# Optimization experiments

Hardware: AMD Instinct MI355X
Metric: run time of the kernel (lower is better)

Reference implementation:

```python
import jax, jax.numpy as jnp
import numpy as np

N = 20000
E = 320000
IN_CH = 512
OUT_CH = 256


def setup_inputs() -> dict:
    key = jax.random.key(0)
    ks = jax.random.split(key, 24)
    p = lambda k, shape: jax.random.normal(k, shape, jnp.float32) * 0.05
    return {
        "x": jax.random.normal(ks[0], (N, IN_CH), jnp.float32),
        "edge_index": jax.random.randint(ks[1], (2, E), 0, N),
        "original_size": 16384,
        "W1": p(ks[2], (IN_CH, 4 * 256)), "as1": p(ks[3], (4, 256)), "ad1": p(ks[4], (4, 256)), "b1": p(ks[5], (1024,)),
        "lw1": p(ks[6], (IN_CH, 1024)), "lb1": p(ks[7], (1024,)),
        "W2": p(ks[8], (1024, 4 * 256)), "as2": p(ks[9], (4, 256)), "ad2": p(ks[10], (4, 256)), "b2": p(ks[11], (1024,)),
        "lw2": p(ks[12], (1024, 1024)), "lb2": p(ks[13], (1024,)),
        "W3": p(ks[14], (1024, 6 * 256)), "as3": p(ks[15], (6, 256)), "ad3": p(ks[16], (6, 256)), "b3": p(ks[17], (256,)),
        "lw3": p(ks[18], (1024, OUT_CH)), "lb3": p(ks[19], (OUT_CH,)),
    }


def gat_conv(x, src, dst, W, a_src, a_dst, bias, heads, ch, concat):
    """PyG-style GATConv: gather -> edge attention -> segment softmax -> scatter-add."""
    n = x.shape[0]
    h = (x @ W).reshape(n, heads, ch)                      # [N,H,C]
    alpha_s = (h * a_src[None]).sum(-1)                    # [N,H]
    alpha_d = (h * a_dst[None]).sum(-1)                    # [N,H]
    e = jax.nn.leaky_relu(alpha_s[src] + alpha_d[dst], 0.2)  # [E,H]
    m = jax.ops.segment_max(e, dst, num_segments=n)        # per-dst max (stable softmax)
    e = jnp.exp(e - m[dst])
    denom = jax.ops.segment_sum(e, dst, num_segments=n)
    alpha = e / (denom[dst] + 1e-16)                       # [E,H]
    msg = h[src] * alpha[:, :, None]                       # [E,H,C]
    out = jax.ops.segment_sum(msg, dst, num_segments=n)    # [N,H,C]
    out = out.reshape(n, heads * ch) if concat else out.mean(axis=1)
    return out + bias


def reference(x, edge_index, original_size, W1, as1, ad1, b1, lw1, lb1,
              W2, as2, ad2, b2, lw2, lb2, W3, as3, ad3, b3, lw3, lb3):
    n = x.shape[0]
    loops = jnp.arange(n)
    src = jnp.concatenate([edge_index[0], loops])  # PyG add_self_loops=True default
    dst = jnp.concatenate([edge_index[1], loops])
    h = jax.nn.elu(gat_conv(x, src, dst, W1, as1, ad1, b1, 4, 256, True) + x @ lw1 + lb1)
    h = jax.nn.elu(gat_conv(h, src, dst, W2, as2, ad2, b2, 4, 256, True) + h @ lw2 + lb2)
    h = gat_conv(h, src, dst, W3, as3, ad3, b3, 6, 256, False) + h @ lw3 + lb3
    return h[:original_size]
```

## Files before the change

### kernel.cpp

```cpp
#include <hip/hip_runtime.h>

#define N_NODES 20000
#define M_PAD   20096
#define E_EDGES 320000

typedef unsigned short u16;
typedef unsigned int   u32;
typedef __attribute__((ext_vector_type(8))) short bf16x8;
typedef __attribute__((ext_vector_type(4))) float f32x4;

__device__ __forceinline__ float bf2f(u16 u){
  u32 x = ((u32)u) << 16; float f; __builtin_memcpy(&f, &x, 4); return f;
}
__device__ __forceinline__ u16 f2bf(float f){
  u32 u; __builtin_memcpy(&u, &f, 4);
  u += 0x7fffu + ((u >> 16) & 1u);
  return (u16)(u >> 16);
}

__device__ __forceinline__ void gl_lds16(const void* g, void* l){
  __builtin_amdgcn_global_load_lds((const __attribute__((address_space(1))) void*)g,
                                   (__attribute__((address_space(3))) void*)l, 16, 0, 0);
}

__global__ void hist_k(const int* __restrict__ ei, int* __restrict__ cnt){
  int i = blockIdx.x * 256 + threadIdx.x;
  if (i < E_EDGES) atomicAdd(&cnt[ei[E_EDGES + i]], 1);
}

__global__ void scan_k(const int* __restrict__ cnt, int* __restrict__ rowp, int n){
  __shared__ int wsum[16], wpre[16];
  __shared__ int carry;
  int tid = threadIdx.x, lane = tid & 63, wv = tid >> 6;
  if (tid == 0) carry = 0;
  __syncthreads();
  for (int base = 0; base < n; base += 1024){
    int i = base + tid;
    int v = (i < n) ? cnt[i] : 0;
    int incl = v;
#pragma unroll
    for (int d = 1; d < 64; d <<= 1){
      int t = __shfl_up(incl, d, 64);
      if (lane >= d) incl += t;
    }
    if (lane == 63) wsum[wv] = incl;
    __syncthreads();
    if (tid == 0){
      int s = carry;
#pragma unroll
      for (int w = 0; w < 16; w++){ wpre[w] = s; s += wsum[w]; }
      carry = s;
    }
    __syncthreads();
    if (i < n) rowp[i] = wpre[wv] + incl - v;
  }
  __syncthreads();
  if (tid == 0) rowp[n] = carry;
}

__global__ void copy_int_k(const int* __restrict__ a, int* __restrict__ b, int n){
  int i = blockIdx.x * 256 + threadIdx.x; if (i < n) b[i] = a[i];
}

__global__ void scatter_k(const int* __restrict__ ei, int* __restrict__ fill, int* __restrict__ esrc){
  int i = blockIdx.x * 256 + threadIdx.x;
  if (i < E_EDGES){
    int d = ei[E_EDGES + i];
    int p = atomicAdd(&fill[d], 1);
    esrc[p] = ei[i];
  }
}

__global__ void tcast_k(const float* __restrict__ src, int Nc, u16* __restrict__ dst, int n0, int ldd){
  __shared__ float tile[32][33];
  int kb = blockIdx.y * 32, nb = blockIdx.x * 32;
  int tx = threadIdx.x, ty = threadIdx.y;
#pragma unroll
  for (int r = 0; r < 32; r += 8)
    tile[ty + r][tx] = src[(size_t)(kb + ty + r) * Nc + nb + tx];
  __syncthreads();
#pragma unroll
  for (int r = 0; r < 32; r += 8){
    int n = nb + ty + r;
    dst[(size_t)(n0 + n) * ldd + kb + tx] = f2bf(tile[tx][ty + r]);
  }
}

__global__ void castx_k(const float* __restrict__ x, u16* __restrict__ o, int realRows){
  int r = blockIdx.x, c = threadIdx.x * 2;
  float2 v = (r < realRows) ? *(const float2*)(x + (size_t)r * 512 + c) : make_float2(0.f, 0.f);
  u32 pk = ((u32)f2bf(v.y) << 16) | (u32)f2bf(v.x);
  *(u32*)(o + (size_t)r * 512 + c) = pk;
}

__global__ void zpad_k(u16* __restrict__ p, int n){
  int i = blockIdx.x * 256 + threadIdx.x; if (i < n) p[i] = 0;
}

__global__ __launch_bounds__(256, 2)
void gemm_bf16(const u16* __restrict__ A, const u16* __restrict__ Bt, u16* __restrict__ C,
               int N, int K)
{
  __shared__ __attribute__((aligned(16))) u16 lA[128 * 32];
  __shared__ __attribute__((aligned(16))) u16 lB[256 * 32];
  const int tid  = threadIdx.x;
  const int wave = tid >> 6, lane = tid & 63;
  const int bn = blockIdx.x, bm = blockIdx.y;
  const int wm = (wave >> 1) * 64, wn = (wave & 1) * 128;

  const int srow  = wave * 16 + (lane >> 2);
  const int skcol = (lane & 3) * 8;
  const u16* Ag0 = A  + (size_t)(bm * 128 + srow) * K + skcol;
  const u16* Ag1 = Ag0 + (size_t)64 * K;
  const u16* Bg  = Bt + (size_t)(bn * 256 + srow) * K + skcol;
  u16* lA0 = lA + wave * 512; u16* lA1 = lA + 2048 + wave * 512;
  u16* lBw = lB + wave * 512;

  f32x4 acc[4][8] = {};

  for (int k0 = 0; k0 < K; k0 += 32){
    gl_lds16(Ag0 + k0, lA0);
    gl_lds16(Ag1 + k0, lA1);
#pragma unroll
    for (int c = 0; c < 4; c++)
      gl_lds16(Bg + (size_t)(c * 64) * K + k0, lBw + c * 2048);
    __syncthreads();
    const int koff = (lane >> 4) * 8;
    const int rsel = lane & 15;
    bf16x8 af[4], bfr[8];
#pragma unroll
    for (int i = 0; i < 4; i++) af[i]  = *(const bf16x8*)&lA[(wm + i * 16 + rsel) * 32 + koff];
#pragma unroll
    for (int j = 0; j < 8; j++) bfr[j] = *(const bf16x8*)&lB[(wn + j * 16 + rsel) * 32 + koff];
#pragma unroll
    for (int i = 0; i < 4; i++)
#pragma unroll
      for (int j = 0; j < 8; j++)
        acc[i][j] = __builtin_amdgcn_mfma_f32_16x16x32_bf16(af[i], bfr[j], acc[i][j], 0, 0, 0);
    __syncthreads();
  }

  const int r0 = (lane >> 4) * 4, cl = lane & 15;
#pragma unroll
  for (int i = 0; i < 4; i++)
#pragma unroll
    for (int j = 0; j < 8; j++){
      int row = bm * 128 + wm + i * 16 + r0;
      int col = bn * 256 + wn + j * 16 + cl;
      u16* cp = C + (size_t)row * N + col;
#pragma unroll
      for (int r = 0; r < 4; r++) cp[(size_t)r * N] = f2bf(acc[i][j][r]);
    }
}

__global__ void alpha_k(const u16* __restrict__ HG, int ldH,
                        const float* __restrict__ a_s, const float* __restrict__ a_d,
                        float* __restrict__ aS, float* __restrict__ aD, int H)
{
  int n = blockIdx.x, h = blockIdx.y, lane = threadIdx.x;
  const u16* rp = HG + (size_t)n * ldH + h * 256 + lane * 4;
  ushort4 u = *(const ushort4*)rp;
  float4 av = *(const float4*)(a_s + h * 256 + lane * 4);
  float4 dv = *(const float4*)(a_d + h * 256 + lane * 4);
  float x0 = bf2f(u.x), x1 = bf2f(u.y), x2 = bf2f(u.z), x3 = bf2f(u.w);
  float s = x0 * av.x + x1 * av.y + x2 * av.z + x3 * av.w;
  float d = x0 * dv.x + x1 * dv.y + x2 * dv.z + x3 * dv.w;
#pragma unroll
  for (int off = 32; off; off >>= 1){ s += __shfl_down(s, off); d += __shfl_down(d, off); }
  if (lane == 0){ aS[(size_t)n * H + h] = s; aD[(size_t)n * H + h] = d; }
}

template<int H, bool FINAL>
__global__ __launch_bounds__(256)
void agg_k(const u16* __restrict__ HG, int ldH,
           const int* __restrict__ rowp, const int* __restrict__ esrc,
           const float* __restrict__ aS, const float* __restrict__ aD,
           const float* __restrict__ bias, const float* __restrict__ lbias,
           int gatCols, u16* __restrict__ outb, int ldo, float* __restrict__ outf)
{
  constexpr int PERT = H;
  constexpr int MAXE = 320;
  __shared__ float s_m[H], s_dinv[H], s_red[4 * H];
  __shared__ float s_ew[MAXE * H];
  __shared__ int   s_src[MAXE];
  __shared__ float s_fin[FINAL ? 1536 : 4];

  const int dst = blockIdx.x;
  const int tid = threadIdx.x, lane = tid & 63, wv = tid >> 6;
  const int e0 = rowp[dst];
  const int deg = rowp[dst + 1] - e0;
  const int nE = deg + 1;
  const bool fits = (nE <= MAXE);

  float adv[H];
#pragma unroll
  for (int h = 0; h < H; h++) adv[h] = aD[(size_t)dst * H + h];

  float lm[H];
#pragma unroll
  for (int h = 0; h < H; h++) lm[h] = -1e30f;
  for (int i = tid; i < nE; i += 256){
    int s = (i == deg) ? dst : esrc[e0 + i];
    if (fits) s_src[i] = s;
#pragma unroll
    for (int h = 0; h < H; h++){
      float e = aS[(size_t)s * H + h] + adv[h];
      e = e > 0.f ? e : 0.2f * e;
      if (fits) s_ew[i * H + h] = e;
      lm[h] = fmaxf(lm[h], e);
    }
  }
#pragma unroll
  for (int h = 0; h < H; h++)
#pragma unroll
    for (int off = 32; off; off >>= 1) lm[h] = fmaxf(lm[h], __shfl_down(lm[h], off));
  if (lane == 0){
#pragma unroll
    for (int h = 0; h < H; h++) s_red[wv * H + h] = lm[h];
  }
  __syncthreads();
  if (tid < H) s_m[tid] = fmaxf(fmaxf(s_red[tid], s_red[H + tid]),
                                fmaxf(s_red[2 * H + tid], s_red[3 * H + tid]));
  __syncthreads();

  float ls[H];
#pragma unroll
  for (int h = 0; h < H; h++) ls[h] = 0.f;
  for (int i = tid; i < nE; i += 256){
    if (fits){
#pragma unroll
      for (int h = 0; h < H; h++){
        float w = __expf(s_ew[i * H + h] - s_m[h]);
        s_ew[i * H + h] = w;
        ls[h] += w;
      }
    } else {
      int s = (i == deg) ? dst : esrc[e0 + i];
#pragma unroll
      for (int h = 0; h < H; h++){
        float e = aS[(size_t)s * H + h] + adv[h];
        e = e > 0.f ? e : 0.2f * e;
        ls[h] += __expf(e - s_m[h]);
      }
    }
  }
#pragma unroll
  for (int h = 0; h < H; h++)
#pragma unroll
    for (int off = 32; off; off >>= 1) ls[h] += __shfl_down(ls[h], off);
  if (lane == 0){
#pragma unroll
    for (int h = 0; h < H; h++) s_red[wv * H + h] = ls[h];
  }
  __syncthreads();
  if (tid < H) s_dinv[tid] = 1.f / (s_red[tid] + s_red[H + tid] + s_red[2 * H + tid] + s_red[3 * H + tid] + 1e-16f);
  __syncthreads();

  float acc[PERT];
#pragma unroll
  for (int c = 0; c < PERT; c++) acc[c] = 0.f;
  const int ch0 = tid * PERT;

  if constexpr (H == 4){
    const int hh = tid >> 6;
    const float dinv = s_dinv[hh];
    const u16* HGb = HG + ch0;
    if (fits){
      int i = 0;
      for (; i + 2 <= nE; i += 2){
        int s0 = s_src[i], s1 = s_src[i + 1];
        float w0 = s_ew[i * 4 + hh] * dinv;
        float w1 = s_ew[i * 4 + 4 + hh] * dinv;
        ushort4 u0 = *(const ushort4*)(HGb + (size_t)s0 * ldH);
        ushort4 u1 = *(const ushort4*)(HGb + (size_t)s1 * ldH);
        acc[0] += w0 * bf2f(u0.x) + w1 * bf2f(u1.x);
        acc[1] += w0 * bf2f(u0.y) + w1 * bf2f(u1.y);
        acc[2] += w0 * bf2f(u0.z) + w1 * bf2f(u1.z);
        acc[3] += w0 * bf2f(u0.w) + w1 * bf2f(u1.w);
      }
      if (i < nE){
        int s0 = s_src[i];
        float w0 = s_ew[i * 4 + hh] * dinv;
        ushort4 u0 = *(const ushort4*)(HGb + (size_t)s0 * ldH);
        acc[0] += w0 * bf2f(u0.x); acc[1] += w0 * bf2f(u0.y);
        acc[2] += w0 * bf2f(u0.z); acc[3] += w0 * bf2f(u0.w);
      }
    } else {
      for (int i = 0; i < nE; i++){
        int s = (i == deg) ? dst : esrc[e0 + i];
        float e = aS[(size_t)s * 4 + hh] + adv[hh];
        e = e > 0.f ? e : 0.2f * e;
        float w = __expf(e - s_m[hh]) * dinv;
        ushort4 u = *(const ushort4*)(HGb + (size_t)s * ldH);
        acc[0] += w * bf2f(u.x); acc[1] += w * bf2f(u.y);
        acc[2] += w * bf2f(u.z); acc[3] += w * bf2f(u.w);
      }
    }
  } else {
    const int h0 = ch0 >> 8;
    const int h1 = (ch0 + 5) >> 8;
    const float dinv0 = s_dinv[h0], dinv1 = s_dinv[h1];
    const int bnd = (h0 + 1) * 256;
    const u32* HGb = (const u32*)HG;
    const int rowd = ldH >> 1;
    if (fits){
      int i = 0;
      for (; i + 2 <= nE; i += 2){
        int s0 = s_src[i], s1 = s_src[i + 1];
        float p0 = s_ew[i * 6 + h0] * dinv0, q0 = s_ew[i * 6 + h1] * dinv1;
        float p1 = s_ew[i * 6 + 6 + h0] * dinv0, q1 = s_ew[i * 6 + 6 + h1] * dinv1;
        const u32* r0p = HGb + (size_t)s0 * rowd + tid * 3;
        const u32* r1p = HGb + (size_t)s1 * rowd + tid * 3;
        u32 a0 = r0p[0], a1 = r0p[1], a2 = r0p[2];
        u32 b0 = r1p[0], b1 = r1p[1], b2 = r1p[2];
        float v0[6] = { bf2f((u16)(a0 & 0xffff)), bf2f((u16)(a0 >> 16)),
                        bf2f((u16)(a1 & 0xffff)), bf2f((u16)(a1 >> 16)),
                        bf2f((u16)(a2 & 0xffff)), bf2f((u16)(a2 >> 16)) };
        float v1[6] = { bf2f((u16)(b0 & 0xffff)), bf2f((u16)(b0 >> 16)),
                        bf2f((u16)(b1 & 0xffff)), bf2f((u16)(b1 >> 16)),
                        bf2f((u16)(b2 & 0xffff)), bf2f((u16)(b2 >> 16)) };
#pragma unroll
        for (int c = 0; c < 6; c++){
          bool lo = (ch0 + c) < bnd;
          acc[c] += (lo ? p0 : q0) * v0[c] + (lo ? p1 : q1) * v1[c];
        }
      }
      if (i < nE){
        int s0 = s_src[i];
        float p0 = s_ew[i * 6 + h0] * dinv0, q0 = s_ew[i * 6 + h1] * dinv1;
        const u32* r0p = HGb + (size_t)s0 * rowd + tid * 3;
        u32 a0 = r0p[0], a1 = r0p[1], a2 = r0p[2];
        float v0[6] = { bf2f((u16)(a0 & 0xffff)), bf2f((u16)(a0 >> 16)),
                        bf2f((u16)(a1 & 0xffff)), bf2f((u16)(a1 >> 16)),
                        bf2f((u16)(a2 & 0xffff)), bf2f((u16)(a2 >> 16)) };
#pragma unroll
        for (int c = 0; c < 6; c++) acc[c] += (((ch0 + c) < bnd) ? p0 : q0) * v0[c];
      }
    } else {
      for (int i = 0; i < nE; i++){
        int s = (i == deg) ? dst : esrc[e0 + i];
        float ea = aS[(size_t)s * 6 + h0] + adv[h0];
        ea = ea > 0.f ? ea : 0.2f * ea;
        float p0 = __expf(ea - s_m[h0]) * dinv0;
        float eb = aS[(size_t)s * 6 + h1] + adv[h1];
        eb = eb > 0.f ? eb : 0.2f * eb;
        float q0 = __expf(eb - s_m[h1]) * dinv1;
        const u32* r0p = HGb + (size_t)s * rowd + tid * 3;
        u32 a0 = r0p[0], a1 = r0p[1], a2 = r0p[2];
        float v0[6] = { bf2f((u16)(a0 & 0xffff)), bf2f((u16)(a0 >> 16)),
                        bf2f((u16)(a1 & 0xffff)), bf2f((u16)(a1 >> 16)),
                        bf2f((u16)(a2 & 0xffff)), bf2f((u16)(a2 >> 16)) };
#pragma unroll
        for (int c = 0; c < 6; c++) acc[c] += (((ch0 + c) < bnd) ? p0 : q0) * v0[c];
      }
    }
  }

  if constexpr (FINAL){
#pragma unroll
    for (int c = 0; c < PERT; c++) s_fin[ch0 + c] = acc[c];
    __syncthreads();
    int c = tid;
    float v = 0.f;
#pragma unroll
    for (int h = 0; h < 6; h++) v += s_fin[h * 256 + c];
    v = v * (1.f / 6.f) + bias[c] + bf2f(HG[(size_t)dst * ldH + gatCols + c]) + lbias[c];
    outf[(size_t)dst * 256 + c] = v;
  } else {
    const u16* lr = HG + (size_t)dst * ldH + gatCols;
    ushort4 u = *(const ushort4*)(lr + ch0);
    float lv[4] = { bf2f(u.x), bf2f(u.y), bf2f(u.z), bf2f(u.w) };
    ushort4 o;
    float v0 = acc[0] + bias[ch0 + 0] + lv[0] + lbias[ch0 + 0]; v0 = v0 > 0.f ? v0 : __expf(v0) - 1.f;
    float v1 = acc[1] + bias[ch0 + 1] + lv[1] + lbias[ch0 + 1]; v1 = v1 > 0.f ? v1 : __expf(v1) - 1.f;
    float v2 = acc[2] + bias[ch0 + 2] + lv[2] + lbias[ch0 + 2]; v2 = v2 > 0.f ? v2 : __expf(v2) - 1.f;
    float v3 = acc[3] + bias[ch0 + 3] + lv[3] + lbias[ch0 + 3]; v3 = v3 > 0.f ? v3 : __expf(v3) - 1.f;
    o.x = f2bf(v0); o.y = f2bf(v1); o.z = f2bf(v2); o.w = f2bf(v3);
    *(ushort4*)(outb + (size_t)dst * ldo + ch0) = o;
  }
}

extern "C" void kernel_launch(void* const* d_in, const int* in_sizes, int n_in,
                              void* d_out, int out_size, void* d_ws, size_t ws_size,
                              hipStream_t stream)
{
  const float* x   = (const float*)d_in[0];
  const int*   ei  = (const int*)  d_in[1];
  const float* W1  = (const float*)d_in[3];
  const float* as1 = (const float*)d_in[4];
  const float* ad1 = (const float*)d_in[5];
  const float* b1  = (const float*)d_in[6];
  const float* lw1 = (const float*)d_in[7];
  const float* lb1 = (const float*)d_in[8];
  const float* W2  = (const float*)d_in[9];
  const float* as2 = (const float*)d_in[10];
  const float* ad2 = (const float*)d_in[11];
  const float* b2  = (const float*)d_in[12];
  const float* lw2 = (const float*)d_in[13];
  const float* lb2 = (const float*)d_in[14];
  const float* W3  = (const float*)d_in[15];
  const float* as3 = (const float*)d_in[16];
  const float* ad3 = (const float*)d_in[17];
  const float* b3  = (const float*)d_in[18];
  const float* lw3 = (const float*)d_in[19];
  const float* lb3 = (const float*)d_in[20];

  char* wp = (char*)d_ws;
  auto nxt = [&](size_t b) -> void* {
    void* p = (void*)wp; wp += (b + 255) & ~(size_t)255; return p;
  };
  u16*  Wt1  = (u16*) nxt((size_t)2048 * 512  * 2);
  u16*  Wt2  = (u16*) nxt((size_t)2048 * 1024 * 2);
  u16*  Wt3  = (u16*) nxt((size_t)1792 * 1024 * 2);
  u16*  Xb   = (u16*) nxt((size_t)M_PAD * 1024 * 2);
  u16*  HG   = (u16*) nxt((size_t)M_PAD * 2048 * 2);
  float* aS  = (float*)nxt((size_t)N_NODES * 6 * 4);
  float* aD  = (float*)nxt((size_t)N_NODES * 6 * 4);
  int*  cnt  = (int*)  nxt((size_t)N_NODES * 4);
  int*  rowp = (int*)  nxt((size_t)(N_NODES + 1) * 4);
  int*  fill = (int*)  nxt((size_t)N_NODES * 4);
  int*  esrc = (int*)  nxt((size_t)E_EDGES * 4);

  hipMemsetAsync(cnt, 0, (size_t)N_NODES * 4, stream);
  hist_k   <<<(E_EDGES + 255) / 256, 256, 0, stream>>>(ei, cnt);
  scan_k   <<<1, 1024, 0, stream>>>(cnt, rowp, N_NODES);
  copy_int_k<<<(N_NODES + 255) / 256, 256, 0, stream>>>(rowp, fill, N_NODES);
  scatter_k<<<(E_EDGES + 255) / 256, 256, 0, stream>>>(ei, fill, esrc);

  dim3 tb(32, 8);
  tcast_k<<<dim3(1024 / 32, 512  / 32), tb, 0, stream>>>(W1,  1024, Wt1, 0,    512);
  tcast_k<<<dim3(1024 / 32, 512  / 32), tb, 0, stream>>>(lw1, 1024, Wt1, 1024, 512);
  tcast_k<<<dim3(1024 / 32, 1024 / 32), tb, 0, stream>>>(W2,  1024, Wt2, 0,    1024);
  tcast_k<<<dim3(1024 / 32, 1024 / 32), tb, 0, stream>>>(lw2, 1024, Wt2, 1024, 1024);
  tcast_k<<<dim3(1536 / 32, 1024 / 32), tb, 0, stream>>>(W3,  1536, Wt3, 0,    1024);
  tcast_k<<<dim3(256  / 32, 1024 / 32), tb, 0, stream>>>(lw3, 256,  Wt3, 1536, 1024);

  castx_k<<<M_PAD, 256, 0, stream>>>(x, Xb, N_NODES);
  zpad_k <<<(96 * 1024 + 255) / 256, 256, 0, stream>>>(Xb + (size_t)N_NODES * 1024, 96 * 1024);

  const int MT = M_PAD / 128;

  gemm_bf16<<<dim3(2048 / 256, MT), 256, 0, stream>>>(Xb, Wt1, HG, 2048, 512);
  alpha_k  <<<dim3(N_NODES, 4), 64, 0, stream>>>(HG, 2048, as1, ad1, aS, aD, 4);
  agg_k<4, false><<<N_NODES, 256, 0, stream>>>(HG, 2048, rowp, esrc, aS, aD, b1, lb1, 1024, Xb, 1024, nullptr);

  gemm_bf16<<<dim3(2048 / 256, MT), 256, 0, stream>>>(Xb, Wt2, HG, 2048, 1024);
  alpha_k  <<<dim3(N_NODES, 4), 64, 0, stream>>>(HG, 2048, as2, ad2, aS, aD, 4);
  agg_k<4, false><<<N_NODES, 256, 0, stream>>>(HG, 2048, rowp, esrc, aS, aD, b2, lb2, 1024, Xb, 1024, nullptr);

  gemm_bf16<<<dim3(1792 / 256, MT), 256, 0, stream>>>(Xb, Wt3, HG, 1792, 1024);
  alpha_k  <<<dim3(N_NODES, 6), 64, 0, stream>>>(HG, 1792, as3, ad3, aS, aD, 6);
  int outRows = out_size / 256;
  agg_k<6, true><<<outRows, 256, 0, stream>>>(HG, 1792, rowp, esrc, aS, aD, b3, lb3, 1536, nullptr, 0, (float*)d_out);

  (void)in_sizes; (void)n_in; (void)ws_size;
}
```

Baseline: 909.1 us.

## Fuse attention-logit dot products into GEMM epilogue and widen aggregation loads

The separate alpha kernel is removed. Attention logits are now computed in the GEMM epilogue from the fp32 accumulators, using a cross-lane shuffle reduction and an LDS combine across waves. The aggregation kernels are rewritten so each thread loads 16-byte chunks of 8 bf16 channels, and two edge groups per block combine partial sums through shared memory. A 384-thread variant handles the six-head layer. The weight transpose launches and the copy kernel are merged into one tcast kernel and the scan, cutting launch count. The GEMM epilogue gains extra LDS work and syncs, and logits now come from unrounded fp32 accumulators rather than bf16-stored values.

```diff
diff --git a/kernel.cpp b/kernel.cpp
--- a/kernel.cpp
+++ b/kernel.cpp
@@ -8,6 +8,7 @@
 typedef unsigned int   u32;
 typedef __attribute__((ext_vector_type(8))) short bf16x8;
 typedef __attribute__((ext_vector_type(4))) float f32x4;
+typedef __attribute__((ext_vector_type(4))) u32   u32x4;
 
 __device__ __forceinline__ float bf2f(u16 u){
   u32 x = ((u32)u) << 16; float f; __builtin_memcpy(&f, &x, 4); return f;
@@ -23,12 +24,22 @@
                                    (__attribute__((address_space(3))) void*)l, 16, 0, 0);
 }
 
+__device__ __forceinline__ void acc8(float* acc, float w, u32x4 p){
+#pragma unroll
+  for (int d = 0; d < 4; d++){
+    u32 u = p[d];
+    acc[2 * d]     += w * bf2f((u16)(u & 0xffff));
+    acc[2 * d + 1] += w * bf2f((u16)(u >> 16));
+  }
+}
+
 __global__ void hist_k(const int* __restrict__ ei, int* __restrict__ cnt){
   int i = blockIdx.x * 256 + threadIdx.x;
   if (i < E_EDGES) atomicAdd(&cnt[ei[E_EDGES + i]], 1);
 }
 
-__global__ void scan_k(const int* __restrict__ cnt, int* __restrict__ rowp, int n){
+__global__ void scan_k(const int* __restrict__ cnt, int* __restrict__ rowp,
+                       int* __restrict__ fill, int n){
   __shared__ int wsum[16], wpre[16];
   __shared__ int carry;
   int tid = threadIdx.x, lane = tid & 63, wv = tid >> 6;
@@ -52,14 +63,10 @@
       carry = s;
     }
     __syncthreads();
-    if (i < n) rowp[i] = wpre[wv] + incl - v;
+    if (i < n){ int e = wpre[wv] + incl - v; rowp[i] = e; fill[i] = e; }
   }
   __syncthreads();
   if (tid == 0) rowp[n] = carry;
-}
-
-__global__ void copy_int_k(const int* __restrict__ a, int* __restrict__ b, int n){
-  int i = blockIdx.x * 256 + threadIdx.x; if (i < n) b[i] = a[i];
 }
 
 __global__ void scatter_k(const int* __restrict__ ei, int* __restrict__ fill, int* __restrict__ esrc){
@@ -71,9 +78,21 @@
   }
 }
 
-__global__ void tcast_k(const float* __restrict__ src, int Nc, u16* __restrict__ dst, int n0, int ldd){
+__global__ void tcast_all(const float* __restrict__ W1, const float* __restrict__ lw1, u16* __restrict__ Wt1,
+                          const float* __restrict__ W2, const float* __restrict__ lw2, u16* __restrict__ Wt2,
+                          const float* __restrict__ W3, const float* __restrict__ lw3, u16* __restrict__ Wt3)
+{
   __shared__ float tile[32][33];
-  int kb = blockIdx.y * 32, nb = blockIdx.x * 32;
+  int b = blockIdx.x;
+  const float* src; u16* dst; int Nc, n0, ldd;
+  if      (b <  512){            src = W1;  Nc = 1024; dst = Wt1; n0 = 0;    ldd = 512;  }
+  else if (b < 1024){ b -=  512; src = lw1; Nc = 1024; dst = Wt1; n0 = 1024; ldd = 512;  }
+  else if (b < 2048){ b -= 1024; src = W2;  Nc = 1024; dst = Wt2; n0 = 0;    ldd = 1024; }
+  else if (b < 3072){ b -= 2048; src = lw2; Nc = 1024; dst = Wt2; n0 = 1024; ldd = 1024; }
+  else if (b < 4608){ b -= 3072; src = W3;  Nc = 1536; dst = Wt3; n0 = 0;    ldd = 1024; }
+  else              { b -= 4608; src = lw3; Nc = 256;  dst = Wt3; n0 = 1536; ldd = 1024; }
+  int gx = Nc / 32;
+  int kb = (b / gx) * 32, nb = (b % gx) * 32;
   int tx = threadIdx.x, ty = threadIdx.y;
 #pragma unroll
   for (int r = 0; r < 32; r += 8)
@@ -99,7 +118,9 @@
 
 __global__ __launch_bounds__(256, 2)
 void gemm_bf16(const u16* __restrict__ A, const u16* __restrict__ Bt, u16* __restrict__ C,
-               int N, int K)
+               int N, int K,
+               const float* __restrict__ a_s, const float* __restrict__ a_d,
+               float* __restrict__ aS, float* __restrict__ aD, int H)
 {
   __shared__ __attribute__((aligned(16))) u16 lA[128 * 32];
   __shared__ __attribute__((aligned(16))) u16 lB[256 * 32];
@@ -151,39 +172,58 @@
 #pragma unroll
       for (int r = 0; r < 4; r++) cp[(size_t)r * N] = f2bf(acc[i][j][r]);
     }
-}
-
-__global__ void alpha_k(const u16* __restrict__ HG, int ldH,
-                        const float* __restrict__ a_s, const float* __restrict__ a_d,
-                        float* __restrict__ aS, float* __restrict__ aD, int H)
+
+  if (bn < H){
+    float* fa = (float*)lA;
+    fa[tid]       = a_s[bn * 256 + tid];
+    fa[256 + tid] = a_d[bn * 256 + tid];
+    __syncthreads();
+    float* fb = (float*)lB;
+    const int q = lane >> 4;
+#pragma unroll
+    for (int i = 0; i < 4; i++)
+#pragma unroll
+      for (int r = 0; r < 4; r++){
+        float ps = 0.f, pd = 0.f;
+#pragma unroll
+        for (int j = 0; j < 8; j++){
+          float v = acc[i][j][r];
+          int c = wn + j * 16 + cl;
+          ps += v * fa[c];
+          pd += v * fa[256 + c];
+        }
+#pragma unroll
+        for (int m = 1; m < 16; m <<= 1){
+          ps += __shfl_xor(ps, m, 64);
+          pd += __shfl_xor(pd, m, 64);
+        }
+        if (cl == 0){
+          int row = wm + i * 16 + q * 4 + r;
+          fb[(wave & 1) * 128 + row]       = ps;
+          fb[256 + (wave & 1) * 128 + row] = pd;
+        }
+      }
+    __syncthreads();
+    if (tid < 128){
+      int row = bm * 128 + tid;
+      aS[(size_t)row * H + bn] = fb[tid] + fb[128 + tid];
+      aD[(size_t)row * H + bn] = fb[256 + tid] + fb[384 + tid];
+    }
+  }
+}
+
+__global__ __launch_bounds__(256)
+void agg4_k(const u16* __restrict__ HG, int ldH,
+            const int* __restrict__ rowp, const int* __restrict__ esrc,
+            const float* __restrict__ aS, const float* __restrict__ aD,
+            const float* __restrict__ bias, const float* __restrict__ lbias,
+            u16* __restrict__ outb)
 {
-  int n = blockIdx.x, h = blockIdx.y, lane = threadIdx.x;
-  const u16* rp = HG + (size_t)n * ldH + h * 256 + lane * 4;
-  ushort4 u = *(const ushort4*)rp;
-  float4 av = *(const float4*)(a_s + h * 256 + lane * 4);
-  float4 dv = *(const float4*)(a_d + h * 256 + lane * 4);
-  float x0 = bf2f(u.x), x1 = bf2f(u.y), x2 = bf2f(u.z), x3 = bf2f(u.w);
-  float s = x0 * av.x + x1 * av.y + x2 * av.z + x3 * av.w;
-  float d = x0 * dv.x + x1 * dv.y + x2 * dv.z + x3 * dv.w;
-#pragma unroll
-  for (int off = 32; off; off >>= 1){ s += __shfl_down(s, off); d += __shfl_down(d, off); }
-  if (lane == 0){ aS[(size_t)n * H + h] = s; aD[(size_t)n * H + h] = d; }
-}
-
-template<int H, bool FINAL>
-__global__ __launch_bounds__(256)
-void agg_k(const u16* __restrict__ HG, int ldH,
-           const int* __restrict__ rowp, const int* __restrict__ esrc,
-           const float* __restrict__ aS, const float* __restrict__ aD,
-           const float* __restrict__ bias, const float* __restrict__ lbias,
-           int gatCols, u16* __restrict__ outb, int ldo, float* __restrict__ outf)
-{
-  constexpr int PERT = H;
   constexpr int MAXE = 320;
-  __shared__ float s_m[H], s_dinv[H], s_red[4 * H];
-  __shared__ float s_ew[MAXE * H];
+  __shared__ float s_m[4], s_dinv[4], s_red[16];
+  __shared__ float s_ew[MAXE * 4];
   __shared__ int   s_src[MAXE];
-  __shared__ float s_fin[FINAL ? 1536 : 4];
+  __shared__ float s_acc[2][1024];
 
   const int dst = blockIdx.x;
   const int tid = threadIdx.x, lane = tid & 63, wv = tid >> 6;
@@ -192,191 +232,259 @@
   const int nE = deg + 1;
   const bool fits = (nE <= MAXE);
 
-  float adv[H];
-#pragma unroll
-  for (int h = 0; h < H; h++) adv[h] = aD[(size_t)dst * H + h];
-
-  float lm[H];
-#pragma unroll
-  for (int h = 0; h < H; h++) lm[h] = -1e30f;
+  float4 adv = *(const float4*)(aD + (size_t)dst * 4);
+
+  float lm[4] = { -1e30f, -1e30f, -1e30f, -1e30f };
   for (int i = tid; i < nE; i += 256){
     int s = (i == deg) ? dst : esrc[e0 + i];
     if (fits) s_src[i] = s;
-#pragma unroll
-    for (int h = 0; h < H; h++){
-      float e = aS[(size_t)s * H + h] + adv[h];
-      e = e > 0.f ? e : 0.2f * e;
-      if (fits) s_ew[i * H + h] = e;
-      lm[h] = fmaxf(lm[h], e);
-    }
-  }
-#pragma unroll
-  for (int h = 0; h < H; h++)
+    float4 as = *(const float4*)(aS + (size_t)s * 4);
+    float e0h = as.x + adv.x; e0h = e0h > 0.f ? e0h : 0.2f * e0h;
+    float e1h = as.y + adv.y; e1h = e1h > 0.f ? e1h : 0.2f * e1h;
+    float e2h = as.z + adv.z; e2h = e2h > 0.f ? e2h : 0.2f * e2h;
+    float e3h = as.w + adv.w; e3h = e3h > 0.f ? e3h : 0.2f * e3h;
+    if (fits){ s_ew[i*4+0]=e0h; s_ew[i*4+1]=e1h; s_ew[i*4+2]=e2h; s_ew[i*4+3]=e3h; }
+    lm[0] = fmaxf(lm[0], e0h); lm[1] = fmaxf(lm[1], e1h);
+    lm[2] = fmaxf(lm[2], e2h); lm[3] = fmaxf(lm[3], e3h);
+  }
+#pragma unroll
+  for (int h = 0; h < 4; h++)
 #pragma unroll
     for (int off = 32; off; off >>= 1) lm[h] = fmaxf(lm[h], __shfl_down(lm[h], off));
   if (lane == 0){
 #pragma unroll
-    for (int h = 0; h < H; h++) s_red[wv * H + h] = lm[h];
-  }
-  __syncthreads();
-  if (tid < H) s_m[tid] = fmaxf(fmaxf(s_red[tid], s_red[H + tid]),
-                                fmaxf(s_red[2 * H + tid], s_red[3 * H + tid]));
-  __syncthreads();
-
-  float ls[H];
-#pragma unroll
-  for (int h = 0; h < H; h++) ls[h] = 0.f;
+    for (int h = 0; h < 4; h++) s_red[wv * 4 + h] = lm[h];
+  }
+  __syncthreads();
+  if (tid < 4) s_m[tid] = fmaxf(fmaxf(s_red[tid], s_red[4 + tid]),
+                                fmaxf(s_red[8 + tid], s_red[12 + tid]));
+  __syncthreads();
+
+  float ls[4] = {0.f, 0.f, 0.f, 0.f};
   for (int i = tid; i < nE; i += 256){
     if (fits){
 #pragma unroll
-      for (int h = 0; h < H; h++){
-        float w = __expf(s_ew[i * H + h] - s_m[h]);
-        s_ew[i * H + h] = w;
+      for (int h = 0; h < 4; h++){
+        float w = __expf(s_ew[i * 4 + h] - s_m[h]);
+        s_ew[i * 4 + h] = w;
         ls[h] += w;
       }
     } else {
       int s = (i == deg) ? dst : esrc[e0 + i];
-#pragma unroll
-      for (int h = 0; h < H; h++){
-        float e = aS[(size_t)s * H + h] + adv[h];
+      float4 as = *(const float4*)(aS + (size_t)s * 4);
+      float e;
+      e = as.x + adv.x; e = e > 0.f ? e : 0.2f * e; ls[0] += __expf(e - s_m[0]);
+      e = as.y + adv.y; e = e > 0.f ? e : 0.2f * e; ls[1] += __expf(e - s_m[1]);
+      e = as.z + adv.z; e = e > 0.f ? e : 0.2f * e; ls[2] += __expf(e - s_m[2]);
+      e = as.w + adv.w; e = e > 0.f ? e : 0.2f * e; ls[3] += __expf(e - s_m[3]);
+    }
+  }
+#pragma unroll
+  for (int h = 0; h < 4; h++)
+#pragma unroll
+    for (int off = 32; off; off >>= 1) ls[h] += __shfl_down(ls[h], off);
+  if (lane == 0){
+#pragma unroll
+    for (int h = 0; h < 4; h++) s_red[wv * 4 + h] = ls[h];
+  }
+  __syncthreads();
+  if (tid < 4) s_dinv[tid] = 1.f / (s_red[tid] + s_red[4 + tid] + s_red[8 + tid] + s_red[12 + tid] + 1e-16f);
+  __syncthreads();
+
+  const int grp = wv >> 1;
+  const int ch0 = (wv & 1) * 512 + lane * 8;
+  const int h   = ch0 >> 8;
+  const float dinv = s_dinv[h];
+  const float mh   = s_m[h];
+  float acc[8] = {};
+  const u16* HGb = HG + ch0;
+
+  if (fits){
+    int i = grp;
+    for (; i + 2 < nE; i += 4){
+      int s0 = s_src[i], s1 = s_src[i + 2];
+      float w0 = s_ew[i * 4 + h] * dinv;
+      float w1 = s_ew[(i + 2) * 4 + h] * dinv;
+      u32x4 p0 = *(const u32x4*)(HGb + (size_t)s0 * ldH);
+      u32x4 p1 = *(const u32x4*)(HGb + (size_t)s1 * ldH);
+      acc8(acc, w0, p0);
+      acc8(acc, w1, p1);
+    }
+    if (i < nE){
+      int s0 = s_src[i];
+      float w0 = s_ew[i * 4 + h] * dinv;
+      u32x4 p0 = *(const u32x4*)(HGb + (size_t)s0 * ldH);
+      acc8(acc, w0, p0);
+    }
+  } else {
+    float advh = aD[(size_t)dst * 4 + h];
+    for (int i = grp; i < nE; i += 2){
+      int s = (i == deg) ? dst : esrc[e0 + i];
+      float e = aS[(size_t)s * 4 + h] + advh;
+      e = e > 0.f ? e : 0.2f * e;
+      float w = __expf(e - mh) * dinv;
+      u32x4 p = *(const u32x4*)(HGb + (size_t)s * ldH);
+      acc8(acc, w, p);
+    }
+  }
+#pragma unroll
+  for (int c = 0; c < 8; c++) s_acc[grp][ch0 + c] = acc[c];
+  __syncthreads();
+
+  const int c4 = tid * 4;
+  const u16* lr = HG + (size_t)dst * ldH + 1024 + c4;
+  ushort4 u = *(const ushort4*)lr;
+  float lv[4] = { bf2f(u.x), bf2f(u.y), bf2f(u.z), bf2f(u.w) };
+  ushort4 o;
+  float v0 = s_acc[0][c4+0] + s_acc[1][c4+0] + bias[c4+0] + lv[0] + lbias[c4+0]; v0 = v0 > 0.f ? v0 : __expf(v0) - 1.f;
+  float v1 = s_acc[0][c4+1] + s_acc[1][c4+1] + bias[c4+1] + lv[1] + lbias[c4+1]; v1 = v1 > 0.f ? v1 : __expf(v1) - 1.f;
+  float v2 = s_acc[0][c4+2] + s_acc[1][c4+2] + bias[c4+2] + lv[2] + lbias[c4+2]; v2 = v2 > 0.f ? v2 : __expf(v2) - 1.f;
+  float v3 = s_acc[0][c4+3] + s_acc[1][c4+3] + bias[c4+3] + lv[3] + lbias[c4+3]; v3 = v3 > 0.f ? v3 : __expf(v3) - 1.f;
+  o.x = f2bf(v0); o.y = f2bf(v1); o.z = f2bf(v2); o.w = f2bf(v3);
+  *(ushort4*)(outb + (size_t)dst * 1024 + c4) = o;
+}
+
+__global__ __launch_bounds__(384)
+void agg6_k(const u16* __restrict__ HG, int ldH,
+            const int* __restrict__ rowp, const int* __restrict__ esrc,
+            const float* __restrict__ aS, const float* __restrict__ aD,
+            const float* __restrict__ bias, const float* __restrict__ lbias,
+            float* __restrict__ outf)
+{
+  constexpr int MAXE = 320;
+  __shared__ float s_m[6], s_dinv[6], s_red[36];
+  __shared__ float s_ew[MAXE * 6];
+  __shared__ int   s_src[MAXE];
+  __shared__ float s_acc[2][1536];
+
+  const int dst = blockIdx.x;
+  const int tid = threadIdx.x, lane = tid & 63, wv = tid >> 6;
+  const int e0 = rowp[dst];
+  const int deg = rowp[dst + 1] - e0;
+  const int nE = deg + 1;
+  const bool fits = (nE <= MAXE);
+
+  float adv[6];
+#pragma unroll
+  for (int h = 0; h < 6; h++) adv[h] = aD[(size_t)dst * 6 + h];
+
+  float lm[6];
+#pragma unroll
+  for (int h = 0; h < 6; h++) lm[h] = -1e30f;
+  for (int i = tid; i < nE; i += 384){
+    int s = (i == deg) ? dst : esrc[e0 + i];
+    if (fits) s_src[i] = s;
+#pragma unroll
+    for (int h = 0; h < 6; h++){
+      float e = aS[(size_t)s * 6 + h] + adv[h];
+      e = e > 0.f ? e : 0.2f * e;
+      if (fits) s_ew[i * 6 + h] = e;
+      lm[h] = fmaxf(lm[h], e);
+    }
+  }
+#pragma unroll
+  for (int h = 0; h < 6; h++)
+#pragma unroll
+    for (int off = 32; off; off >>= 1) lm[h] = fmaxf(lm[h], __shfl_down(lm[h], off));
+  if (lane == 0){
+#pragma unroll
+    for (int h = 0; h < 6; h++) s_red[wv * 6 + h] = lm[h];
+  }
+  __syncthreads();
+  if (tid < 6){
+    float m = s_red[tid];
+#pragma unroll
+    for (int w = 1; w < 6; w++) m = fmaxf(m, s_red[w * 6 + tid]);
+    s_m[tid] = m;
+  }
+  __syncthreads();
+
+  float ls[6];
+#pragma unroll
+  for (int h = 0; h < 6; h++) ls[h] = 0.f;
+  for (int i = tid; i < nE; i += 384){
+    if (fits){
+#pragma unroll
+      for (int h = 0; h < 6; h++){
+        float w = __expf(s_ew[i * 6 + h] - s_m[h]);
+        s_ew[i * 6 + h] = w;
+        ls[h] += w;
+      }
+    } else {
+      int s = (i == deg) ? dst : esrc[e0 + i];
+#pragma unroll
+      for (int h = 0; h < 6; h++){
+        float e = aS[(size_t)s * 6 + h] + adv[h];
         e = e > 0.f ? e : 0.2f * e;
         ls[h] += __expf(e - s_m[h]);
       }
     }
   }
 #pragma unroll
-  for (int h = 0; h < H; h++)
+  for (int h = 0; h < 6; h++)
 #pragma unroll
     for (int off = 32; off; off >>= 1) ls[h] += __shfl_down(ls[h], off);
   if (lane == 0){
 #pragma unroll
-    for (int h = 0; h < H; h++) s_red[wv * H + h] = ls[h];
-  }
-  __syncthreads();
-  if (tid < H) s_dinv[tid] = 1.f / (s_red[tid] + s_red[H + tid] + s_red[2 * H + tid] + s_red[3 * H + tid] + 1e-16f);
-  __syncthreads();
-
-  float acc[PERT];
-#pragma unroll
-  for (int c = 0; c < PERT; c++) acc[c] = 0.f;
-  const int ch0 = tid * PERT;
-
-  if constexpr (H == 4){
-    const int hh = tid >> 6;
-    const float dinv = s_dinv[hh];
-    const u16* HGb = HG + ch0;
-    if (fits){
-      int i = 0;
-      for (; i + 2 <= nE; i += 2){
-        int s0 = s_src[i], s1 = s_src[i + 1];
-        float w0 = s_ew[i * 4 + hh] * dinv;
-        float w1 = s_ew[i * 4 + 4 + hh] * dinv;
-        ushort4 u0 = *(const ushort4*)(HGb + (size_t)s0 * ldH);
-        ushort4 u1 = *(const ushort4*)(HGb + (size_t)s1 * ldH);
-        acc[0] += w0 * bf2f(u0.x) + w1 * bf2f(u1.x);
-        acc[1] += w0 * bf2f(u0.y) + w1 * bf2f(u1.y);
-        acc[2] += w0 * bf2f(u0.z) + w1 * bf2f(u1.z);
-        acc[3] += w0 * bf2f(u0.w) + w1 * bf2f(u1.w);
-      }
-      if (i < nE){
-        int s0 = s_src[i];
-        float w0 = s_ew[i * 4 + hh] * dinv;
-        ushort4 u0 = *(const ushort4*)(HGb + (size_t)s0 * ldH);
-        acc[0] += w0 * bf2f(u0.x); acc[1] += w0 * bf2f(u0.y);
-        acc[2] += w0 * bf2f(u0.z); acc[3] += w0 * bf2f(u0.w);
-      }
-    } else {
-      for (int i = 0; i < nE; i++){
-        int s = (i == deg) ? dst : esrc[e0 + i];
-        float e = aS[(size_t)s * 4 + hh] + adv[hh];
-        e = e > 0.f ? e : 0.2f * e;
-        float w = __expf(e - s_m[hh]) * dinv;
-        ushort4 u = *(const ushort4*)(HGb + (size_t)s * ldH);
-        acc[0] += w * bf2f(u.x); acc[1] += w * bf2f(u.y);
-        acc[2] += w * bf2f(u.z); acc[3] += w * bf2f(u.w);
-      }
+    for (int h = 0; h < 6; h++) s_red[wv * 6 + h] = ls[h];
+  }
+  __syncthreads();
+  if (tid < 6){
+    float s = 0.f;
+#pragma unroll
+    for (int w = 0; w < 6; w++) s += s_red[w * 6 + tid];
+    s_dinv[tid] = 1.f / (s + 1e-16f);
+  }
+  __syncthreads();
+
+  const int grp  = wv / 3;
+  const int wrow = wv - grp * 3;
+  const int ch0  = wrow * 512 + lane * 8;
+  const int h    = ch0 >> 8;
+  const float dinv = s_dinv[h];
+  const float mh   = s_m[h];
+  float acc[8] = {};
+  const u16* HGb = HG + ch0;
+
+  if (fits){
+    int i = grp;
+    for (; i + 2 < nE; i += 4){
+      int s0 = s_src[i], s1 = s_src[i + 2];
+      float w0 = s_ew[i * 6 + h] * dinv;
+      float w1 = s_ew[(i + 2) * 6 + h] * dinv;
+      u32x4 p0 = *(const u32x4*)(HGb + (size_t)s0 * ldH);
+      u32x4 p1 = *(const u32x4*)(HGb + (size_t)s1 * ldH);
+      acc8(acc, w0, p0);
+      acc8(acc, w1, p1);
+    }
+    if (i < nE){
+      int s0 = s_src[i];
+      float w0 = s_ew[i * 6 + h] * dinv;
+      u32x4 p0 = *(const u32x4*)(HGb + (size_t)s0 * ldH);
+      acc8(acc, w0, p0);
     }
   } else {
-    const int h0 = ch0 >> 8;
-    const int h1 = (ch0 + 5) >> 8;
-    const float dinv0 = s_dinv[h0], dinv1 = s_dinv[h1];
-    const int bnd = (h0 + 1) * 256;
-    const u32* HGb = (const u32*)HG;
-    const int rowd = ldH >> 1;
-    if (fits){
-      int i = 0;
-      for (; i + 2 <= nE; i += 2){
-        int s0 = s_src[i], s1 = s_src[i + 1];
-        float p0 = s_ew[i * 6 + h0] * dinv0, q0 = s_ew[i * 6 + h1] * dinv1;
-        float p1 = s_ew[i * 6 + 6 + h0] * dinv0, q1 = s_ew[i * 6 + 6 + h1] * dinv1;
-        const u32* r0p = HGb + (size_t)s0 * rowd + tid * 3;
-        const u32* r1p = HGb + (size_t)s1 * rowd + tid * 3;
-        u32 a0 = r0p[0], a1 = r0p[1], a2 = r0p[2];
-        u32 b0 = r1p[0], b1 = r1p[1], b2 = r1p[2];
-        float v0[6] = { bf2f((u16)(a0 & 0xffff)), bf2f((u16)(a0 >> 16)),
-                        bf2f((u16)(a1 & 0xffff)), bf2f((u16)(a1 >> 16)),
-                        bf2f((u16)(a2 & 0xffff)), bf2f((u16)(a2 >> 16)) };
-        float v1[6] = { bf2f((u16)(b0 & 0xffff)), bf2f((u16)(b0 >> 16)),
-                        bf2f((u16)(b1 & 0xffff)), bf2f((u16)(b1 >> 16)),
-                        bf2f((u16)(b2 & 0xffff)), bf2f((u16)(b2 >> 16)) };
-#pragma unroll
-        for (int c = 0; c < 6; c++){
-          bool lo = (ch0 + c) < bnd;
-          acc[c] += (lo ? p0 : q0) * v0[c] + (lo ? p1 : q1) * v1[c];
-        }
-      }
-      if (i < nE){
-        int s0 = s_src[i];
-        float p0 = s_ew[i * 6 + h0] * dinv0, q0 = s_ew[i * 6 + h1] * dinv1;
-        const u32* r0p = HGb + (size_t)s0 * rowd + tid * 3;
-        u32 a0 = r0p[0], a1 = r0p[1], a2 = r0p[2];
-        float v0[6] = { bf2f((u16)(a0 & 0xffff)), bf2f((u16)(a0 >> 16)),
-                        bf2f((u16)(a1 & 0xffff)), bf2f((u16)(a1 >> 16)),
-                        bf2f((u16)(a2 & 0xffff)), bf2f((u16)(a2 >> 16)) };
-#pragma unroll
-        for (int c = 0; c < 6; c++) acc[c] += (((ch0 + c) < bnd) ? p0 : q0) * v0[c];
-      }
-    } else {
-      for (int i = 0; i < nE; i++){
-        int s = (i == deg) ? dst : esrc[e0 + i];
-        float ea = aS[(size_t)s * 6 + h0] + adv[h0];
-        ea = ea > 0.f ? ea : 0.2f * ea;
-        float p0 = __expf(ea - s_m[h0]) * dinv0;
-        float eb = aS[(size_t)s * 6 + h1] + adv[h1];
-        eb = eb > 0.f ? eb : 0.2f * eb;
-        float q0 = __expf(eb - s_m[h1]) * dinv1;
-        const u32* r0p = HGb + (size_t)s * rowd + tid * 3;
-        u32 a0 = r0p[0], a1 = r0p[1], a2 = r0p[2];
-        float v0[6] = { bf2f((u16)(a0 & 0xffff)), bf2f((u16)(a0 >> 16)),
-                        bf2f((u16)(a1 & 0xffff)), bf2f((u16)(a1 >> 16)),
-                        bf2f((u16)(a2 & 0xffff)), bf2f((u16)(a2 >> 16)) };
-#pragma unroll
-        for (int c = 0; c < 6; c++) acc[c] += (((ch0 + c) < bnd) ? p0 : q0) * v0[c];
-      }
-    }
-  }
-
-  if constexpr (FINAL){
-#pragma unroll
-    for (int c = 0; c < PERT; c++) s_fin[ch0 + c] = acc[c];
-    __syncthreads();
+    float advh = aD[(size_t)dst * 6 + h];
+    for (int i = grp; i < nE; i += 2){
+      int s = (i == deg) ? dst : esrc[e0 + i];
+      float e = aS[(size_t)s * 6 + h] + advh;
+      e = e > 0.f ? e : 0.2f * e;
+      float w = __expf(e - mh) * dinv;
+      u32x4 p = *(const u32x4*)(HGb + (size_t)s * ldH);
+      acc8(acc, w, p);
+    }
+  }
+#pragma unroll
+  for (int c = 0; c < 8; c++) s_acc[grp][ch0 + c] = acc[c];
+  __syncthreads();
+
+  if (tid < 256){
     int c = tid;
     float v = 0.f;
 #pragma unroll
-    for (int h = 0; h < 6; h++) v += s_fin[h * 256 + c];
-    v = v * (1.f / 6.f) + bias[c] + bf2f(HG[(size_t)dst * ldH + gatCols + c]) + lbias[c];
+    for (int hh = 0; hh < 6; hh++) v += s_acc[0][hh * 256 + c] + s_acc[1][hh * 256 + c];
+    v = v * (1.f / 6.f) + bias[c] + bf2f(HG[(size_t)dst * ldH + 1536 + c]) + lbias[c];
     outf[(size_t)dst * 256 + c] = v;
-  } else {
-    const u16* lr = HG + (size_t)dst * ldH + gatCols;
-    ushort4 u = *(const ushort4*)(lr + ch0);
-    float lv[4] = { bf2f(u.x), bf2f(u.y), bf2f(u.z), bf2f(u.w) };
-    ushort4 o;
-    float v0 = acc[0] + bias[ch0 + 0] + lv[0] + lbias[ch0 + 0]; v0 = v0 > 0.f ? v0 : __expf(v0) - 1.f;
-    float v1 = acc[1] + bias[ch0 + 1] + lv[1] + lbias[ch0 + 1]; v1 = v1 > 0.f ? v1 : __expf(v1) - 1.f;
-    float v2 = acc[2] + bias[ch0 + 2] + lv[2] + lbias[ch0 + 2]; v2 = v2 > 0.f ? v2 : __expf(v2) - 1.f;
-    float v3 = acc[3] + bias[ch0 + 3] + lv[3] + lbias[ch0 + 3]; v3 = v3 > 0.f ? v3 : __expf(v3) - 1.f;
-    o.x = f2bf(v0); o.y = f2bf(v1); o.z = f2bf(v2); o.w = f2bf(v3);
-    *(ushort4*)(outb + (size_t)dst * ldo + ch0) = o;
   }
 }
 
@@ -414,8 +522,8 @@
   u16*  Wt3  = (u16*) nxt((size_t)1792 * 1024 * 2);
   u16*  Xb   = (u16*) nxt((size_t)M_PAD * 1024 * 2);
   u16*  HG   = (u16*) nxt((size_t)M_PAD * 2048 * 2);
-  float* aS  = (float*)nxt((size_t)N_NODES * 6 * 4);
-  float* aD  = (float*)nxt((size_t)N_NODES * 6 * 4);
+  float* aS  = (float*)nxt((size_t)M_PAD * 6 * 4);
+  float* aD  = (float*)nxt((size_t)M_PAD * 6 * 4);
   int*  cnt  = (int*)  nxt((size_t)N_NODES * 4);
   int*  rowp = (int*)  nxt((size_t)(N_NODES + 1) * 4);
   int*  fill = (int*)  nxt((size_t)N_NODES * 4);
@@ -423,35 +531,25 @@
 
   hipMemsetAsync(cnt, 0, (size_t)N_NODES * 4, stream);
   hist_k   <<<(E_EDGES + 255) / 256, 256, 0, stream>>>(ei, cnt);
-  scan_k   <<<1, 1024, 0, stream>>>(cnt, rowp, N_NODES);
-  copy_int_k<<<(N_NODES + 255) / 256, 256, 0, stream>>>(rowp, fill, N_NODES);
+  scan_k   <<<1, 1024, 0, stream>>>(cnt, rowp, fill, N_NODES);
   scatter_k<<<(E_EDGES + 255) / 256, 256, 0, stream>>>(ei, fill, esrc);
 
-  dim3 tb(32, 8);
-  tcast_k<<<dim3(1024 / 32, 512  / 32), tb, 0, stream>>>(W1,  1024, Wt1, 0,    512);
-  tcast_k<<<dim3(1024 / 32, 512  / 32), tb, 0, stream>>>(lw1, 1024, Wt1, 1024, 512);
-  tcast_k<<<dim3(1024 / 32, 1024 / 32), tb, 0, stream>>>(W2,  1024, Wt2, 0,    1024);
-  tcast_k<<<dim3(1024 / 32, 1024 / 32), tb, 0, stream>>>(lw2, 1024, Wt2, 1024, 1024);
-  tcast_k<<<dim3(1536 / 32, 1024 / 32), tb, 0, stream>>>(W3,  1536, Wt3, 0,    1024);
-  tcast_k<<<dim3(256  / 32, 1024 / 32), tb, 0, stream>>>(lw3, 256,  Wt3, 1536, 1024);
+  tcast_all<<<4864, dim3(32, 8), 0, stream>>>(W1, lw1, Wt1, W2, lw2, Wt2, W3, lw3, Wt3);
 
   castx_k<<<M_PAD, 256, 0, stream>>>(x, Xb, N_NODES);
   zpad_k <<<(96 * 1024 + 255) / 256, 256, 0, stream>>>(Xb + (size_t)N_NODES * 1024, 96 * 1024);
 
   const int MT = M_PAD / 128;
 
-  gemm_bf16<<<dim3(2048 / 256, MT), 256, 0, stream>>>(Xb, Wt1, HG, 2048, 512);
-  alpha_k  <<<dim3(N_NODES, 4), 64, 0, stream>>>(HG, 2048, as1, ad1, aS, aD, 4);
-  agg_k<4, false><<<N_NODES, 256, 0, stream>>>(HG, 2048, rowp, esrc, aS, aD, b1, lb1, 1024, Xb, 1024, nullptr);
-
-  gemm_bf16<<<dim3(2048 / 256, MT), 256, 0, stream>>>(Xb, Wt2, HG, 2048, 1024);
-  alpha_k  <<<dim3(N_NODES, 4), 64, 0, stream>>>(HG, 2048, as2, ad2, aS, aD, 4);
-  agg_k<4, false><<<N_NODES, 256, 0, stream>>>(HG, 2048, rowp, esrc, aS, aD, b2, lb2, 1024, Xb, 1024, nullptr);
-
-  gemm_bf16<<<dim3(1792 / 256, MT), 256, 0, stream>>>(Xb, Wt3, HG, 1792, 1024);
-  alpha_k  <<<dim3(N_NODES, 6), 64, 0, stream>>>(HG, 1792, as3, ad3, aS, aD, 6);
+  gemm_bf16<<<dim3(2048 / 256, MT), 256, 0, stream>>>(Xb, Wt1, HG, 2048, 512,  as1, ad1, aS, aD, 4);
+  agg4_k   <<<N_NODES, 256, 0, stream>>>(HG, 2048, rowp, esrc, aS, aD, b1, lb1, Xb);
+
+  gemm_bf16<<<dim3(2048 / 256, MT), 256, 0, stream>>>(Xb, Wt2, HG, 2048, 1024, as2, ad2, aS, aD, 4);
+  agg4_k   <<<N_NODES, 256, 0, stream>>>(HG, 2048, rowp, esrc, aS, aD, b2, lb2, Xb);
+
+  gemm_bf16<<<dim3(1792 / 256, MT), 256, 0, stream>>>(Xb, Wt3, HG, 1792, 1024, as3, ad3, aS, aD, 6);
   int outRows = out_size / 256;
-  agg_k<6, true><<<outRows, 256, 0, stream>>>(HG, 1792, rowp, esrc, aS, aD, b3, lb3, 1536, nullptr, 0, (float*)d_out);
+  agg6_k   <<<outRows, 384, 0, stream>>>(HG, 1792, rowp, esrc, aS, aD, b3, lb3, (float*)d_out);
 
   (void)in_sizes; (void)n_in; (void)ws_size;
 }
```

New measurement: 873.7 us. 3.9% less time.
